# Kernel tuning notes

Measured on AMD Instinct MI355X. Metric: run time of the kernel, lower is better.

## Reference

```python
import jax, jax.numpy as jnp
import numpy as np

THRESHOLD = 1.0

@jax.custom_vjp
def spike(u):
    # Heaviside fire with snntorch ATan surrogate gradient (alpha=2.0)
    return (u > 0).astype(u.dtype)

def _spike_fwd(u):
    return spike(u), u

def _spike_bwd(u, g):
    # d/du atan surrogate: (alpha/2) / (1 + (pi/2*alpha*u)^2) with alpha=2 -> 1/(1+(pi*u)^2)
    return (g / (1.0 + (jnp.pi * u) ** 2),)

spike.defvjp(_spike_fwd, _spike_bwd)


def setup_inputs() -> dict:
    key = jax.random.key(0)
    k1, k2, k3, k4 = jax.random.split(key, 4)
    B, D, M = 1024, 256, 256
    x = jax.random.normal(k1, (B, D), dtype=jnp.float32)
    mem_states = jax.random.normal(k2, (M, B, D), dtype=jnp.float32)
    # mode_selector Linear(D -> M)
    W = jax.random.normal(k3, (M, D), dtype=jnp.float32) / np.sqrt(D)
    b = jax.random.normal(k4, (M,), dtype=jnp.float32) * 0.01
    return {"x": x, "mem_states": mem_states, "W": W, "b": b}


def reference(x, mem_states, W, b):
    M = mem_states.shape[0]
    # gating scores: [B, M]
    mode_scores = jax.nn.softmax(x @ W.T + b, axis=-1)
    # snn.Leaky(beta=i) for i in range(M): beta is the integer loop index
    betas = jnp.arange(M, dtype=x.dtype)[:, None, None]  # [M,1,1]
    # subtract-reset uses detached spike of the incoming membrane
    reset = jax.lax.stop_gradient((mem_states - THRESHOLD > 0).astype(x.dtype))
    mem_new = betas * mem_states + x[None, :, :] - reset * THRESHOLD  # [M,B,D]
    spk = spike(mem_new - THRESHOLD)  # [M,B,D]
    # faithful to source broadcast: [M,B,D] * [1,B,M] (requires D == M), sum over modes
    mixed = (spk * mode_scores[None, :, :]).sum(axis=0)  # [B,D]
    return mixed, mem_new, mode_scores
```

## Files before the change

kernel.cpp:

```cpp
#include <hip/hip_runtime.h>

#define THRESH 1.0f

typedef float fvec4 __attribute__((ext_vector_type(4)));

__device__ __forceinline__ float rl(float v, int l) {
    return __int_as_float(__builtin_amdgcn_readlane(__float_as_int(v), l));
}

__global__ __launch_bounds__(256) void transpose_kernel(
    const float* __restrict__ W, float* __restrict__ Wt, int M, int D)
{
    __shared__ float tile[32][33];
    const int tilesK = D / 32;
    const int bx = blockIdx.x % tilesK;
    const int by = blockIdx.x / tilesK;
    const int lx = threadIdx.x & 31;
    const int ly = threadIdx.x >> 5;
    #pragma unroll
    for (int j = 0; j < 4; ++j)
        tile[ly + j * 8][lx] = W[(size_t)(by * 32 + ly + j * 8) * D + bx * 32 + lx];
    __syncthreads();
    #pragma unroll
    for (int j = 0; j < 4; ++j)
        Wt[(size_t)(bx * 32 + ly + j * 8) * M + by * 32 + lx] = tile[lx][ly + j * 8];
}

__global__ __launch_bounds__(256) void row_kernel(
    const float* __restrict__ x, const float* __restrict__ mem,
    const float* __restrict__ Wt, const float* __restrict__ bias,
    float* __restrict__ mem_new, float* __restrict__ scores,
    float* __restrict__ mixed, int plane4)
{
    const int b    = blockIdx.x;
    const int tid  = threadIdx.x;
    const int wave = tid >> 6;
    const int lane = tid & 63;
    const int q    = wave;
    const int p    = lane;
    const int pos4 = b * 64 + p;

    __shared__ __align__(16) float sc_f[256];
    __shared__ fvec4 cnt_lds[4][64];
    __shared__ float wredm[4];
    __shared__ float wreds[4];

    const fvec4* mem4 = reinterpret_cast<const fvec4*>(mem);
    fvec4* out4       = reinterpret_cast<fvec4*>(mem_new);
    const fvec4 xv    = reinterpret_cast<const fvec4*>(x)[pos4];

    float cx = 0.f, cy = 0.f, cz = 0.f, cw = 0.f;

    auto step = [&](int m) {
        const float bm = (float)m;
        const size_t off = (size_t)m * plane4 + pos4;
        const fvec4 mv = __builtin_nontemporal_load(&mem4[off]);
        fvec4 nv;
        nv.x = __fsub_rn(__fadd_rn(__fmul_rn(bm, mv.x), xv.x),
                         (mv.x - THRESH > 0.f) ? THRESH : 0.f);
        nv.y = __fsub_rn(__fadd_rn(__fmul_rn(bm, mv.y), xv.y),
                         (mv.y - THRESH > 0.f) ? THRESH : 0.f);
        nv.z = __fsub_rn(__fadd_rn(__fmul_rn(bm, mv.z), xv.z),
                         (mv.z - THRESH > 0.f) ? THRESH : 0.f);
        nv.w = __fsub_rn(__fadd_rn(__fmul_rn(bm, mv.w), xv.w),
                         (mv.w - THRESH > 0.f) ? THRESH : 0.f);
        __builtin_nontemporal_store(nv, &out4[off]);
        cx += (nv.x - THRESH > 0.f) ? 1.f : 0.f;
        cy += (nv.y - THRESH > 0.f) ? 1.f : 0.f;
        cz += (nv.z - THRESH > 0.f) ? 1.f : 0.f;
        cw += (nv.w - THRESH > 0.f) ? 1.f : 0.f;
    };

    auto prologue = [&]() {
        const fvec4 xq = reinterpret_cast<const fvec4*>(x)[(size_t)b * 64 + lane];
        float a0 = 0.f;
        #pragma unroll 4
        for (int j = 0; j < 64; ++j) {
            const float w0 = Wt[(size_t)(4 * j + 0) * 256 + tid];
            const float w1 = Wt[(size_t)(4 * j + 1) * 256 + tid];
            const float w2 = Wt[(size_t)(4 * j + 2) * 256 + tid];
            const float w3 = Wt[(size_t)(4 * j + 3) * 256 + tid];
            a0 = fmaf(w0, rl(xq.x, j), a0);
            a0 = fmaf(w1, rl(xq.y, j), a0);
            a0 = fmaf(w2, rl(xq.z, j), a0);
            a0 = fmaf(w3, rl(xq.w, j), a0);
        }
        const float l = a0 + bias[tid];

        float mx = l;
        #pragma unroll
        for (int off = 32; off; off >>= 1) mx = fmaxf(mx, __shfl_xor(mx, off, 64));
        if (lane == 0) wredm[wave] = mx;
        __syncthreads();
        mx = fmaxf(fmaxf(wredm[0], wredm[1]), fmaxf(wredm[2], wredm[3]));

        const float e = expf(l - mx);
        float s = e;
        #pragma unroll
        for (int off = 32; off; off >>= 1) s += __shfl_xor(s, off, 64);
        if (lane == 0) wreds[wave] = s;
        __syncthreads();
        const float tot = wreds[0] + wreds[1] + wreds[2] + wreds[3];

        const float sc = e / tot;
        sc_f[tid] = sc;
        scores[(size_t)b * 256 + tid] = sc;
    };

    const int mstart = q * 64;

    if (((blockIdx.x >> 3) & 1) == 0) {
        #pragma unroll 8
        for (int m = mstart; m < mstart + 32; ++m) step(m);
        prologue();
        #pragma unroll 8
        for (int m = mstart + 32; m < mstart + 64; ++m) step(m);
    } else {
        prologue();
        #pragma unroll 8
        for (int m = mstart; m < mstart + 64; ++m) step(m);
    }

    fvec4 cv; cv.x = cx; cv.y = cy; cv.z = cz; cv.w = cw;
    cnt_lds[q][p] = cv;
    __syncthreads();

    if (q == 0) {
        const fvec4 c0 = cnt_lds[0][p];
        const fvec4 c1 = cnt_lds[1][p];
        const fvec4 c2 = cnt_lds[2][p];
        const fvec4 c3 = cnt_lds[3][p];
        fvec4 c;
        c.x = (c0.x + c1.x) + (c2.x + c3.x);
        c.y = (c0.y + c1.y) + (c2.y + c3.y);
        c.z = (c0.z + c1.z) + (c2.z + c3.z);
        c.w = (c0.w + c1.w) + (c2.w + c3.w);
        const fvec4 sc = reinterpret_cast<const fvec4*>(sc_f)[p];
        fvec4 r;
        r.x = sc.x * c.x; r.y = sc.y * c.y;
        r.z = sc.z * c.z; r.w = sc.w * c.w;
        reinterpret_cast<fvec4*>(mixed)[pos4] = r;
    }
}

__global__ __launch_bounds__(256) void scores_kernel_fb(
    const float* __restrict__ x, const float* __restrict__ W,
    const float* __restrict__ bias, float* __restrict__ scores,
    int D, int M)
{
    const int b = blockIdx.x;
    __shared__ __align__(16) float x_lds[256];
    __shared__ float logits[256];
    __shared__ float wred[4];
    const int tid  = threadIdx.x;
    const int wave = tid >> 6;
    const int lane = tid & 63;
    x_lds[tid] = x[(size_t)b * D + tid];
    __syncthreads();
    const float4* W4 = reinterpret_cast<const float4*>(W);
    const float4  xv = reinterpret_cast<const float4*>(x_lds)[lane];
    for (int i = 0; i < 64; ++i) {
        const int m = wave * 64 + i;
        const float4 wv = W4[(size_t)m * 64 + lane];
        float pp = wv.x * xv.x + wv.y * xv.y + wv.z * xv.z + wv.w * xv.w;
        #pragma unroll
        for (int off = 32; off; off >>= 1) pp += __shfl_xor(pp, off, 64);
        if (lane == 0) logits[m] = pp + bias[m];
    }
    __syncthreads();
    float l = logits[tid];
    float mx = l;
    #pragma unroll
    for (int off = 32; off; off >>= 1) mx = fmaxf(mx, __shfl_xor(mx, off, 64));
    if (lane == 0) wred[wave] = mx;
    __syncthreads();
    mx = fmaxf(fmaxf(wred[0], wred[1]), fmaxf(wred[2], wred[3]));
    __syncthreads();
    const float e = expf(l - mx);
    float s = e;
    #pragma unroll
    for (int off = 32; off; off >>= 1) s += __shfl_xor(s, off, 64);
    if (lane == 0) wred[wave] = s;
    __syncthreads();
    const float tot = wred[0] + wred[1] + wred[2] + wred[3];
    scores[(size_t)b * M + tid] = e / tot;
}

__global__ __launch_bounds__(256) void neuron_kernel_fb(
    const float* __restrict__ x, const float* __restrict__ mem,
    const float* __restrict__ scores, float* __restrict__ mixed,
    float* __restrict__ mem_new, int M, int plane4)
{
    const int idx = blockIdx.x * 256 + threadIdx.x;
    if (idx >= plane4) return;
    const float4* x4   = reinterpret_cast<const float4*>(x);
    const float4* mem4 = reinterpret_cast<const float4*>(mem);
    const float4* sc4  = reinterpret_cast<const float4*>(scores);
    float4* out4       = reinterpret_cast<float4*>(mem_new);
    float4* mix4       = reinterpret_cast<float4*>(mixed);
    const float4 xv = x4[idx];
    float cx = 0.f, cy = 0.f, cz = 0.f, cw = 0.f;
    #pragma unroll 4
    for (int m = 0; m < M; ++m) {
        const float bm = (float)m;
        const size_t off = (size_t)m * plane4 + idx;
        const float4 mv = mem4[off];
        float4 nv;
        nv.x = __fsub_rn(__fadd_rn(__fmul_rn(bm, mv.x), xv.x),
                         (mv.x - THRESH > 0.f) ? THRESH : 0.f);
        nv.y = __fsub_rn(__fadd_rn(__fmul_rn(bm, mv.y), xv.y),
                         (mv.y - THRESH > 0.f) ? THRESH : 0.f);
        nv.z = __fsub_rn(__fadd_rn(__fmul_rn(bm, mv.z), xv.z),
                         (mv.z - THRESH > 0.f) ? THRESH : 0.f);
        nv.w = __fsub_rn(__fadd_rn(__fmul_rn(bm, mv.w), xv.w),
                         (mv.w - THRESH > 0.f) ? THRESH : 0.f);
        out4[off] = nv;
        cx += (nv.x - THRESH > 0.f) ? 1.f : 0.f;
        cy += (nv.y - THRESH > 0.f) ? 1.f : 0.f;
        cz += (nv.z - THRESH > 0.f) ? 1.f : 0.f;
        cw += (nv.w - THRESH > 0.f) ? 1.f : 0.f;
    }
    const float4 sc = sc4[idx];
    float4 mx;
    mx.x = sc.x * cx; mx.y = sc.y * cy; mx.z = sc.z * cz; mx.w = sc.w * cw;
    mix4[idx] = mx;
}

extern "C" void kernel_launch(void* const* d_in, const int* in_sizes, int n_in,
                              void* d_out, int out_size, void* d_ws, size_t ws_size,
                              hipStream_t stream) {
    const float* x    = (const float*)d_in[0];
    const float* mem  = (const float*)d_in[1];
    const float* W    = (const float*)d_in[2];
    const float* bias = (const float*)d_in[3];

    const int M = in_sizes[3];
    const int D = in_sizes[2] / M;
    const int B = in_sizes[0] / D;
    const int plane  = B * D;
    const int plane4 = plane / 4;

    float* out_mixed  = (float*)d_out;
    float* out_mem    = out_mixed + plane;
    float* out_scores = out_mem + (size_t)M * plane;

    const size_t wt_bytes = (size_t)M * D * sizeof(float);

    const bool shapes_ok = (D == 256) && (M == 256);

    if (shapes_ok && ws_size >= wt_bytes) {
        float* Wt = (float*)d_ws;
        transpose_kernel<<<(M / 32) * (D / 32), 256, 0, stream>>>(W, Wt, M, D);
        row_kernel<<<B, 256, 0, stream>>>(
            x, mem, Wt, bias, out_mem, out_scores, out_mixed, plane4);
    } else {
        scores_kernel_fb<<<B, 256, 0, stream>>>(x, W, bias, out_scores, D, M);
        neuron_kernel_fb<<<(plane4 + 255) / 256, 256, 0, stream>>>(
            x, mem, out_scores, out_mixed, out_mem, M, plane4);
    }
}
```

Before: 121.5 us.

## Process two batch rows per 512-thread block with prefetched membrane loads

Replaces the one-row 256-thread kernel with a 512-thread kernel that handles two batch rows, each half computing one row's softmax scores. Four membrane loads are issued before the gating GEMV so their memory latency overlaps the score computation. The old per-block staggering of the prologue is removed. The 512-thread blocks need more LDS and registers, and the block-wide syncs now stall all eight waves together.

```diff
diff --git a/kernel.cpp b/kernel.cpp
--- a/kernel.cpp
+++ b/kernel.cpp
@@ -26,35 +26,81 @@
         Wt[(size_t)(bx * 32 + ly + j * 8) * M + by * 32 + lx] = tile[lx][ly + j * 8];
 }
 
-__global__ __launch_bounds__(256) void row_kernel(
+__global__ __launch_bounds__(512, 4) void rowpair512_kernel(
     const float* __restrict__ x, const float* __restrict__ mem,
     const float* __restrict__ Wt, const float* __restrict__ bias,
     float* __restrict__ mem_new, float* __restrict__ scores,
     float* __restrict__ mixed, int plane4)
 {
-    const int b    = blockIdx.x;
+    const int b0   = blockIdx.x * 2;
     const int tid  = threadIdx.x;
-    const int wave = tid >> 6;
     const int lane = tid & 63;
-    const int q    = wave;
-    const int p    = lane;
-    const int pos4 = b * 64 + p;
-
-    __shared__ __align__(16) float sc_f[256];
-    __shared__ fvec4 cnt_lds[4][64];
-    __shared__ float wredm[4];
-    __shared__ float wreds[4];
+    const int half = tid >> 8;
+    const int htid = tid & 255;
+    const int w4   = (tid >> 6) & 3;
+
+    const int q    = tid >> 7;
+    const int pp   = tid & 127;
+    const int pos4 = b0 * 64 + pp;
+
+    __shared__ __align__(16) float sc_lds[2][256];
+    __shared__ fvec4 cnt_lds[4][128];
+    __shared__ float wredm[2][4];
+    __shared__ float wreds[2][4];
 
     const fvec4* mem4 = reinterpret_cast<const fvec4*>(mem);
     fvec4* out4       = reinterpret_cast<fvec4*>(mem_new);
-    const fvec4 xv    = reinterpret_cast<const fvec4*>(x)[pos4];
-
+
+    const int mstart = q * 64;
+    const fvec4 pf0 = __builtin_nontemporal_load(&mem4[(size_t)(mstart + 0) * plane4 + pos4]);
+    const fvec4 pf1 = __builtin_nontemporal_load(&mem4[(size_t)(mstart + 1) * plane4 + pos4]);
+    const fvec4 pf2 = __builtin_nontemporal_load(&mem4[(size_t)(mstart + 2) * plane4 + pos4]);
+    const fvec4 pf3 = __builtin_nontemporal_load(&mem4[(size_t)(mstart + 3) * plane4 + pos4]);
+
+    {
+        const fvec4 xq = reinterpret_cast<const fvec4*>(x)[(size_t)(b0 + half) * 64 + lane];
+        float a0 = 0.f;
+        #pragma unroll 4
+        for (int j = 0; j < 64; ++j) {
+            const float w0 = Wt[(size_t)(4 * j + 0) * 256 + htid];
+            const float w1 = Wt[(size_t)(4 * j + 1) * 256 + htid];
+            const float w2 = Wt[(size_t)(4 * j + 2) * 256 + htid];
+            const float w3 = Wt[(size_t)(4 * j + 3) * 256 + htid];
+            a0 = fmaf(w0, rl(xq.x, j), a0);
+            a0 = fmaf(w1, rl(xq.y, j), a0);
+            a0 = fmaf(w2, rl(xq.z, j), a0);
+            a0 = fmaf(w3, rl(xq.w, j), a0);
+        }
+        const float l = a0 + bias[htid];
+
+        float mx = l;
+        #pragma unroll
+        for (int off = 32; off; off >>= 1) mx = fmaxf(mx, __shfl_xor(mx, off, 64));
+        if (lane == 0) wredm[half][w4] = mx;
+        __syncthreads();
+        mx = fmaxf(fmaxf(wredm[half][0], wredm[half][1]),
+                   fmaxf(wredm[half][2], wredm[half][3]));
+
+        const float e = expf(l - mx);
+        float s = e;
+        #pragma unroll
+        for (int off = 32; off; off >>= 1) s += __shfl_xor(s, off, 64);
+        if (lane == 0) wreds[half][w4] = s;
+        __syncthreads();
+        const float tot = wreds[half][0] + wreds[half][1] +
+                          wreds[half][2] + wreds[half][3];
+
+        const float sc = e / tot;
+        sc_lds[half][htid] = sc;
+        scores[(size_t)(b0 + half) * 256 + htid] = sc;
+    }
+
+    const fvec4 xv = reinterpret_cast<const fvec4*>(x)[pos4];
     float cx = 0.f, cy = 0.f, cz = 0.f, cw = 0.f;
 
-    auto step = [&](int m) {
+    auto process = [&](const fvec4 mv, int m) {
         const float bm = (float)m;
         const size_t off = (size_t)m * plane4 + pos4;
-        const fvec4 mv = __builtin_nontemporal_load(&mem4[off]);
         fvec4 nv;
         nv.x = __fsub_rn(__fadd_rn(__fmul_rn(bm, mv.x), xv.x),
                          (mv.x - THRESH > 0.f) ? THRESH : 0.f);
@@ -71,71 +117,33 @@
         cw += (nv.w - THRESH > 0.f) ? 1.f : 0.f;
     };
 
-    auto prologue = [&]() {
-        const fvec4 xq = reinterpret_cast<const fvec4*>(x)[(size_t)b * 64 + lane];
-        float a0 = 0.f;
-        #pragma unroll 4
-        for (int j = 0; j < 64; ++j) {
-            const float w0 = Wt[(size_t)(4 * j + 0) * 256 + tid];
-            const float w1 = Wt[(size_t)(4 * j + 1) * 256 + tid];
-            const float w2 = Wt[(size_t)(4 * j + 2) * 256 + tid];
-            const float w3 = Wt[(size_t)(4 * j + 3) * 256 + tid];
-            a0 = fmaf(w0, rl(xq.x, j), a0);
-            a0 = fmaf(w1, rl(xq.y, j), a0);
-            a0 = fmaf(w2, rl(xq.z, j), a0);
-            a0 = fmaf(w3, rl(xq.w, j), a0);
-        }
-        const float l = a0 + bias[tid];
-
-        float mx = l;
-        #pragma unroll
-        for (int off = 32; off; off >>= 1) mx = fmaxf(mx, __shfl_xor(mx, off, 64));
-        if (lane == 0) wredm[wave] = mx;
-        __syncthreads();
-        mx = fmaxf(fmaxf(wredm[0], wredm[1]), fmaxf(wredm[2], wredm[3]));
-
-        const float e = expf(l - mx);
-        float s = e;
-        #pragma unroll
-        for (int off = 32; off; off >>= 1) s += __shfl_xor(s, off, 64);
-        if (lane == 0) wreds[wave] = s;
-        __syncthreads();
-        const float tot = wreds[0] + wreds[1] + wreds[2] + wreds[3];
-
-        const float sc = e / tot;
-        sc_f[tid] = sc;
-        scores[(size_t)b * 256 + tid] = sc;
-    };
-
-    const int mstart = q * 64;
-
-    if (((blockIdx.x >> 3) & 1) == 0) {
-        #pragma unroll 8
-        for (int m = mstart; m < mstart + 32; ++m) step(m);
-        prologue();
-        #pragma unroll 8
-        for (int m = mstart + 32; m < mstart + 64; ++m) step(m);
-    } else {
-        prologue();
-        #pragma unroll 8
-        for (int m = mstart; m < mstart + 64; ++m) step(m);
+    process(pf0, mstart + 0);
+    process(pf1, mstart + 1);
+    process(pf2, mstart + 2);
+    process(pf3, mstart + 3);
+
+    #pragma unroll 8
+    for (int mm = 4; mm < 64; ++mm) {
+        const int m = mstart + mm;
+        const fvec4 mv = __builtin_nontemporal_load(&mem4[(size_t)m * plane4 + pos4]);
+        process(mv, m);
     }
 
     fvec4 cv; cv.x = cx; cv.y = cy; cv.z = cz; cv.w = cw;
-    cnt_lds[q][p] = cv;
+    cnt_lds[q][pp] = cv;
     __syncthreads();
 
     if (q == 0) {
-        const fvec4 c0 = cnt_lds[0][p];
-        const fvec4 c1 = cnt_lds[1][p];
-        const fvec4 c2 = cnt_lds[2][p];
-        const fvec4 c3 = cnt_lds[3][p];
+        const fvec4 c0 = cnt_lds[0][pp];
+        const fvec4 c1 = cnt_lds[1][pp];
+        const fvec4 c2 = cnt_lds[2][pp];
+        const fvec4 c3 = cnt_lds[3][pp];
         fvec4 c;
         c.x = (c0.x + c1.x) + (c2.x + c3.x);
         c.y = (c0.y + c1.y) + (c2.y + c3.y);
         c.z = (c0.z + c1.z) + (c2.z + c3.z);
         c.w = (c0.w + c1.w) + (c2.w + c3.w);
-        const fvec4 sc = reinterpret_cast<const fvec4*>(sc_f)[p];
+        const fvec4 sc = reinterpret_cast<const fvec4*>(sc_lds[pp >> 6])[pp & 63];
         fvec4 r;
         r.x = sc.x * c.x; r.y = sc.y * c.y;
         r.z = sc.z * c.z; r.w = sc.w * c.w;
@@ -246,12 +254,12 @@
 
     const size_t wt_bytes = (size_t)M * D * sizeof(float);
 
-    const bool shapes_ok = (D == 256) && (M == 256);
+    const bool shapes_ok = (D == 256) && (M == 256) && (B % 2 == 0);
 
     if (shapes_ok && ws_size >= wt_bytes) {
         float* Wt = (float*)d_ws;
         transpose_kernel<<<(M / 32) * (D / 32), 256, 0, stream>>>(W, Wt, M, D);
-        row_kernel<<<B, 256, 0, stream>>>(
+        rowpair512_kernel<<<B / 2, 512, 0, stream>>>(
             x, mem, Wt, bias, out_mem, out_scores, out_mixed, plane4);
     } else {
         scores_kernel_fb<<<B, 256, 0, stream>>>(x, W, bias, out_scores, D, M);
```

Result: faster. 109.1 us (-10.2%).
